# Performance work log

Hardware: AMD Instinct MI355X
Metric: run time of the kernel (lower is better)

## Reference

```python
import jax, jax.numpy as jnp
import numpy as np

# FPMA (Mitchell-style) approximate bf16 multiply: a*b is approximated by
# integer-adding the exponent+mantissa bit fields of the two bf16 operands
# and subtracting the exponent bias offset (0x3F80 for bf16). Sign is XOR of
# sign bits. Underflow is flushed to zero; overflow clamped to max finite.
SIGN_MASK = 0x8000
MAG_MASK = 0x7FFF
BIAS_OFF = 0x3F80  # 127 << 7 (bf16 exponent bias in bit position)
MAX_FINITE = 0x7F7F
CHUNK = 4  # rows of the input processed per scan step (bounds the [C,N,K] intermediate)


def _fpma_matmul(x, w):
    """x: [M,K] bf16, w: [N,K] bf16 -> [M,N] fp32 accumulated approximate products."""
    xb = jax.lax.bitcast_convert_type(x, jnp.uint16).astype(jnp.int32)  # [M,K]
    wb = jax.lax.bitcast_convert_type(w, jnp.uint16).astype(jnp.int32)  # [N,K]
    M, K = xb.shape
    xs, xm = xb & SIGN_MASK, xb & MAG_MASK
    ws, wm = wb & SIGN_MASK, wb & MAG_MASK

    def block(args):
        bs, bm = args  # each [CHUNK, K]
        sign = bs[:, None, :] ^ ws[None]                      # [C,N,K]
        mag = bm[:, None, :] + wm[None] - BIAS_OFF            # approx exp+mant add
        mag = jnp.clip(mag, 0, MAX_FINITE)                    # flush underflow, clamp overflow
        is_zero = (bm[:, None, :] == 0) | (wm[None] == 0)     # exact-zero operands
        bits = jnp.where(is_zero, 0, sign | mag).astype(jnp.uint16)
        prod = jax.lax.bitcast_convert_type(bits, jnp.bfloat16)
        return prod.astype(jnp.float32).sum(-1)               # [C,N] fp32 accumulate

    xs_c = xs.reshape(M // CHUNK, CHUNK, K)
    xm_c = xm.reshape(M // CHUNK, CHUNK, K)
    out = jax.lax.map(block, (xs_c, xm_c))                    # [M//C, C, N]
    return out.reshape(M, -1)


def setup_inputs() -> dict:
    key = jax.random.key(0)
    k1, k2, k3 = jax.random.split(key, 3)
    M, K, N = 4096, 2048, 2048
    input = jax.random.normal(k1, (M, K), dtype=jnp.bfloat16)
    weight = (jax.random.normal(k2, (N, K), dtype=jnp.float32) * 0.02).astype(jnp.bfloat16)
    bias = (jax.random.normal(k3, (1, N), dtype=jnp.float32) * 0.02).astype(jnp.bfloat16)
    return {"input": input, "weight": weight, "bias": bias}


def reference(input, weight, bias):
    orig_shape = input.shape[:-1]
    x = input.reshape(-1, input.shape[-1])
    acc = _fpma_matmul(x, weight)                 # [M,N] fp32
    out = acc.astype(jnp.bfloat16) + bias         # bias added in bf16, as in the kernel wrapper
    return out.reshape(*orig_shape, weight.shape[0])
```

## Files before the change

### kernel.cpp

```cpp
#include <hip/hip_runtime.h>
#include <stdint.h>

typedef unsigned short v2u   __attribute__((ext_vector_type(2)));
typedef unsigned short u16x8 __attribute__((ext_vector_type(8)));
typedef short          s16x8 __attribute__((ext_vector_type(8)));
typedef float          f32x4 __attribute__((ext_vector_type(4)));

#define TM 64
#define TN 64
#define BK 32

__device__ __forceinline__ uint32_t rnd_bf16(float f) {
    uint32_t u = __builtin_bit_cast(uint32_t, f);
    return (u + 0x7FFFu + ((u >> 16) & 1u)) >> 16;
}
__device__ __forceinline__ float bf16_to_f32(uint32_t bits16) {
    return __builtin_bit_cast(float, bits16 << 16);
}

__device__ __forceinline__ uint32_t pack_x(uint32_t w0, uint32_t w1) {
    uint32_t u = (w0 >> 16) | (w1 & 0xFFFF0000u);
    const v2u vfloor = {0x2000, 0x2000};
    v2u m = __builtin_bit_cast(v2u, u & 0x7FFF7FFFu);
    m = __builtin_elementwise_max(m, vfloor);
    uint32_t c = (u & 0x80008000u) ^ 0xC080C080u;
    v2u xp = m + __builtin_bit_cast(v2u, c);
    return __builtin_bit_cast(uint32_t, xp);
}
__device__ __forceinline__ uint32_t pack_w(uint32_t w0, uint32_t w1) {
    uint32_t v = (w0 >> 16) | (w1 & 0xFFFF0000u);
    const v2u vfloor = {0x2000, 0x2000};
    v2u m = __builtin_bit_cast(v2u, v & 0x7FFF7FFFu);
    m = __builtin_elementwise_max(m, vfloor);
    return __builtin_bit_cast(uint32_t, m) | (v & 0x80008000u);
}

__global__ __launch_bounds__(256, 2)
void fpma_gemm(const uint32_t* __restrict__ X,
               const uint32_t* __restrict__ Wt,
               const float*    __restrict__ Bias,
               float* __restrict__ Out,
               int M, int N, int K)
{
    __shared__ uint32_t Xp[2][64 * 16];
    __shared__ uint32_t Wp[2][64 * 16];

    const int tid  = threadIdx.x;
    const int lane = tid & 63;
    const int warp = tid >> 6;
    const int wm = warp >> 1, wn = warp & 1;
    const int m0 = blockIdx.y * TM;
    const int n0 = blockIdx.x * TN;

    const int cc = lane & 15;
    const int q  = lane >> 4;
    const int mi = cc >> 2;
    const int ni = cc & 3;

    const int xrd = (32 * wm + mi) * 16 + ((q ^ mi) << 2);
    int wrd[4];
    #pragma unroll
    for (int t = 0; t < 4; ++t)
        wrd[t] = (32 * wn + ni) * 16 + ((q ^ ni) << 2) + (((q + t) & 3) << 6);

    u16x8 bt[4];
    #pragma unroll
    for (int t = 0; t < 4; ++t) {
        unsigned short v = ((cc >> 2) == ((q + t) & 3)) ? (unsigned short)0x3F80
                                                        : (unsigned short)0;
        bt[t] = (u16x8){v, v, v, v, v, v, v, v};
    }

    const int srow = tid >> 2;
    const int soct = tid & 3;
    const uint32_t* xptr = X  + (size_t)(m0 + srow) * K + soct * 8;
    const uint32_t* wptr = Wt + (size_t)(n0 + srow) * K + soct * 8;
    const int st = srow * 16 + ((soct ^ (srow & 3)) << 2);

    f32x4 acc[8][2];
    #pragma unroll
    for (int a = 0; a < 8; ++a)
        #pragma unroll
        for (int bg = 0; bg < 2; ++bg) acc[a][bg] = (f32x4){0.f, 0.f, 0.f, 0.f};

    {
        uint4 a0 = *(const uint4*)(xptr), a1 = *(const uint4*)(xptr + 4);
        uint4 b0 = *(const uint4*)(wptr), b1 = *(const uint4*)(wptr + 4);
        uint4 px = {pack_x(a0.x, a0.y), pack_x(a0.z, a0.w),
                    pack_x(a1.x, a1.y), pack_x(a1.z, a1.w)};
        uint4 pw = {pack_w(b0.x, b0.y), pack_w(b0.z, b0.w),
                    pack_w(b1.x, b1.y), pack_w(b1.z, b1.w)};
        *(uint4*)&Xp[0][st] = px;
        *(uint4*)&Wp[0][st] = pw;
    }
    uint4 gx0 = {0,0,0,0}, gx1 = {0,0,0,0}, gw0 = {0,0,0,0}, gw1 = {0,0,0,0};
    const int ksteps = K / BK;
    if (ksteps > 1) {
        xptr += BK; wptr += BK;
        gx0 = *(const uint4*)(xptr); gx1 = *(const uint4*)(xptr + 4);
        gw0 = *(const uint4*)(wptr); gw1 = *(const uint4*)(wptr + 4);
    }
    __syncthreads();

    #pragma unroll 1
    for (int kt = 0; kt < ksteps; ++kt) {
        const int cur = kt & 1;
        if (kt + 1 < ksteps) {
            uint4 px = {pack_x(gx0.x, gx0.y), pack_x(gx0.z, gx0.w),
                        pack_x(gx1.x, gx1.y), pack_x(gx1.z, gx1.w)};
            uint4 pw = {pack_w(gw0.x, gw0.y), pack_w(gw0.z, gw0.w),
                        pack_w(gw1.x, gw1.y), pack_w(gw1.z, gw1.w)};
            *(uint4*)&Xp[cur ^ 1][st] = px;
            *(uint4*)&Wp[cur ^ 1][st] = pw;
            if (kt + 2 < ksteps) {
                xptr += BK; wptr += BK;
                gx0 = *(const uint4*)(xptr); gx1 = *(const uint4*)(xptr + 4);
                gw0 = *(const uint4*)(wptr); gw1 = *(const uint4*)(wptr + 4);
            }
        }

        u16x8 xf[8];
        #pragma unroll
        for (int a = 0; a < 8; ++a)
            xf[a] = __builtin_bit_cast(u16x8,
                        *(const uint4*)&Xp[cur][xrd + a * 64]);

        #pragma unroll
        for (int bg = 0; bg < 2; ++bg) {
            u16x8 wf[4];
            #pragma unroll
            for (int t = 0; t < 4; ++t)
                wf[t] = __builtin_bit_cast(u16x8,
                            *(const uint4*)&Wp[cur][wrd[t] + bg * 256]);
            #pragma unroll
            for (int t = 0; t < 4; ++t)
                #pragma unroll
                for (int a = 0; a < 8; ++a) {
                    u16x8 p = xf[a] + wf[t];
                    acc[a][bg] = __builtin_amdgcn_mfma_f32_16x16x32_bf16(
                        __builtin_bit_cast(s16x8, p),
                        __builtin_bit_cast(s16x8, bt[t]),
                        acc[a][bg], 0, 0, 0);
                }
        }
        __syncthreads();
    }

    const int g = cc >> 2;
    f32x4 bias_[2];
    #pragma unroll
    for (int bg = 0; bg < 2; ++bg)
        bias_[bg] = *(const f32x4*)&Bias[n0 + 32 * wn + 16 * bg + 4 * g];

    #pragma unroll
    for (int a = 0; a < 8; ++a) {
        if ((cc & 3) == (a & 3)) {
            #pragma unroll
            for (int bg = 0; bg < 2; ++bg) {
                float o[4];
                #pragma unroll
                for (int j = 0; j < 4; ++j)
                    o[j] = bf16_to_f32(rnd_bf16(
                               bf16_to_f32(rnd_bf16(acc[a][bg][j])) + bias_[bg][j]));
                const size_t row = (size_t)(m0 + 32 * wm + 4 * a + q) * N;
                *(float4*)&Out[row + n0 + 32 * wn + 16 * bg + 4 * g] =
                    make_float4(o[0], o[1], o[2], o[3]);
            }
        }
    }
}

extern "C" void kernel_launch(void* const* d_in, const int* in_sizes, int n_in,
                              void* d_out, int out_size, void* d_ws, size_t ws_size,
                              hipStream_t stream) {
    (void)n_in; (void)d_ws; (void)ws_size; (void)out_size;
    const uint32_t* X = (const uint32_t*)d_in[0];
    const uint32_t* W = (const uint32_t*)d_in[1];
    const float*    B = (const float*)d_in[2];
    float* O = (float*)d_out;

    int N = in_sizes[2];
    int K = (N > 0) ? in_sizes[1] / N : 0;
    int M = (K > 0) ? in_sizes[0] / K : 0;
    if (N <= 0 || K <= 0 || M <= 0 ||
        (long long)N * K != (long long)in_sizes[1] ||
        (long long)M * K != (long long)in_sizes[0] ||
        (M % TM) || (N % TN) || (K % BK)) {
        M = 4096; K = 2048; N = 2048;
    }

    dim3 grid(N / TN, M / TM);
    fpma_gemm<<<grid, 256, 0, stream>>>(X, W, B, O, M, N, K);
}
```

Before: 558.1 us.

## Split k-step into four barrier-separated phases interleaving LDS staging with MFMA bursts

```diff
diff --git a/kernel.cpp b/kernel.cpp
--- a/kernel.cpp
+++ b/kernel.cpp
@@ -33,6 +33,10 @@
     v2u m = __builtin_bit_cast(v2u, v & 0x7FFF7FFFu);
     m = __builtin_elementwise_max(m, vfloor);
     return __builtin_bit_cast(uint32_t, m) | (v & 0x80008000u);
+}
+
+__device__ __forceinline__ void lgkm0() {
+    asm volatile("s_waitcnt lgkmcnt(0)" ::: "memory");
 }
 
 __global__ __launch_bounds__(256, 2)
@@ -86,12 +90,10 @@
     {
         uint4 a0 = *(const uint4*)(xptr), a1 = *(const uint4*)(xptr + 4);
         uint4 b0 = *(const uint4*)(wptr), b1 = *(const uint4*)(wptr + 4);
-        uint4 px = {pack_x(a0.x, a0.y), pack_x(a0.z, a0.w),
-                    pack_x(a1.x, a1.y), pack_x(a1.z, a1.w)};
-        uint4 pw = {pack_w(b0.x, b0.y), pack_w(b0.z, b0.w),
-                    pack_w(b1.x, b1.y), pack_w(b1.z, b1.w)};
-        *(uint4*)&Xp[0][st] = px;
-        *(uint4*)&Wp[0][st] = pw;
+        *(uint4*)&Xp[0][st] = (uint4){pack_x(a0.x,a0.y), pack_x(a0.z,a0.w),
+                                      pack_x(a1.x,a1.y), pack_x(a1.z,a1.w)};
+        *(uint4*)&Wp[0][st] = (uint4){pack_w(b0.x,b0.y), pack_w(b0.z,b0.w),
+                                      pack_w(b1.x,b1.y), pack_w(b1.z,b1.w)};
     }
     uint4 gx0 = {0,0,0,0}, gx1 = {0,0,0,0}, gw0 = {0,0,0,0}, gw1 = {0,0,0,0};
     const int ksteps = K / BK;
@@ -102,49 +104,78 @@
     }
     __syncthreads();
 
+#define PHASE_MFMA(T, WA, WB)                                             \
+    __builtin_amdgcn_s_setprio(1);                                        \
+    _Pragma("unroll")                                                     \
+    for (int a = 0; a < 8; ++a) {                                         \
+        u16x8 p = xf[a] + (WA);                                           \
+        acc[a][0] = __builtin_amdgcn_mfma_f32_16x16x32_bf16(              \
+            __builtin_bit_cast(s16x8, p),                                 \
+            __builtin_bit_cast(s16x8, bt[T]), acc[a][0], 0, 0, 0);        \
+    }                                                                     \
+    _Pragma("unroll")                                                     \
+    for (int a = 0; a < 8; ++a) {                                         \
+        u16x8 p = xf[a] + (WB);                                           \
+        acc[a][1] = __builtin_amdgcn_mfma_f32_16x16x32_bf16(              \
+            __builtin_bit_cast(s16x8, p),                                 \
+            __builtin_bit_cast(s16x8, bt[T]), acc[a][1], 0, 0, 0);        \
+    }                                                                     \
+    __builtin_amdgcn_s_setprio(0);
+
     #pragma unroll 1
     for (int kt = 0; kt < ksteps; ++kt) {
         const int cur = kt & 1;
-        if (kt + 1 < ksteps) {
-            uint4 px = {pack_x(gx0.x, gx0.y), pack_x(gx0.z, gx0.w),
-                        pack_x(gx1.x, gx1.y), pack_x(gx1.z, gx1.w)};
-            uint4 pw = {pack_w(gw0.x, gw0.y), pack_w(gw0.z, gw0.w),
-                        pack_w(gw1.x, gw1.y), pack_w(gw1.z, gw1.w)};
-            *(uint4*)&Xp[cur ^ 1][st] = px;
-            *(uint4*)&Wp[cur ^ 1][st] = pw;
-            if (kt + 2 < ksteps) {
-                xptr += BK; wptr += BK;
-                gx0 = *(const uint4*)(xptr); gx1 = *(const uint4*)(xptr + 4);
-                gw0 = *(const uint4*)(wptr); gw1 = *(const uint4*)(wptr + 4);
-            }
-        }
-
+        const bool stage = (kt + 1 < ksteps);
+        const bool pre   = (kt + 2 < ksteps);
         u16x8 xf[8];
+
         #pragma unroll
         for (int a = 0; a < 8; ++a)
             xf[a] = __builtin_bit_cast(u16x8,
                         *(const uint4*)&Xp[cur][xrd + a * 64]);
-
-        #pragma unroll
-        for (int bg = 0; bg < 2; ++bg) {
-            u16x8 wf[4];
-            #pragma unroll
-            for (int t = 0; t < 4; ++t)
-                wf[t] = __builtin_bit_cast(u16x8,
-                            *(const uint4*)&Wp[cur][wrd[t] + bg * 256]);
-            #pragma unroll
-            for (int t = 0; t < 4; ++t)
-                #pragma unroll
-                for (int a = 0; a < 8; ++a) {
-                    u16x8 p = xf[a] + wf[t];
-                    acc[a][bg] = __builtin_amdgcn_mfma_f32_16x16x32_bf16(
-                        __builtin_bit_cast(s16x8, p),
-                        __builtin_bit_cast(s16x8, bt[t]),
-                        acc[a][bg], 0, 0, 0);
-                }
+        u16x8 w0a = __builtin_bit_cast(u16x8, *(const uint4*)&Wp[cur][wrd[0]]);
+        u16x8 w0b = __builtin_bit_cast(u16x8, *(const uint4*)&Wp[cur][wrd[0] + 256]);
+        if (stage)
+            *(uint4*)&Xp[cur ^ 1][st] = (uint4){pack_x(gx0.x,gx0.y), pack_x(gx0.z,gx0.w),
+                                                pack_x(gx1.x,gx1.y), pack_x(gx1.z,gx1.w)};
+        __builtin_amdgcn_s_barrier();
+        lgkm0();
+        PHASE_MFMA(0, w0a, w0b)
+        __builtin_amdgcn_s_barrier();
+
+        u16x8 w1a = __builtin_bit_cast(u16x8, *(const uint4*)&Wp[cur][wrd[1]]);
+        u16x8 w1b = __builtin_bit_cast(u16x8, *(const uint4*)&Wp[cur][wrd[1] + 256]);
+        if (stage)
+            *(uint4*)&Wp[cur ^ 1][st] = (uint4){pack_w(gw0.x,gw0.y), pack_w(gw0.z,gw0.w),
+                                                pack_w(gw1.x,gw1.y), pack_w(gw1.z,gw1.w)};
+        __builtin_amdgcn_s_barrier();
+        lgkm0();
+        PHASE_MFMA(1, w1a, w1b)
+        __builtin_amdgcn_s_barrier();
+
+        u16x8 w2a = __builtin_bit_cast(u16x8, *(const uint4*)&Wp[cur][wrd[2]]);
+        u16x8 w2b = __builtin_bit_cast(u16x8, *(const uint4*)&Wp[cur][wrd[2] + 256]);
+        if (pre) {
+            xptr += BK;
+            gx0 = *(const uint4*)(xptr); gx1 = *(const uint4*)(xptr + 4);
         }
-        __syncthreads();
-    }
+        __builtin_amdgcn_s_barrier();
+        lgkm0();
+        PHASE_MFMA(2, w2a, w2b)
+        __builtin_amdgcn_s_barrier();
+
+        u16x8 w3a = __builtin_bit_cast(u16x8, *(const uint4*)&Wp[cur][wrd[3]]);
+        u16x8 w3b = __builtin_bit_cast(u16x8, *(const uint4*)&Wp[cur][wrd[3] + 256]);
+        if (pre) {
+            wptr += BK;
+            gw0 = *(const uint4*)(wptr); gw1 = *(const uint4*)(wptr + 4);
+        }
+        __builtin_amdgcn_s_barrier();
+        lgkm0();
+        PHASE_MFMA(3, w3a, w3b)
+        __builtin_amdgcn_s_barrier();
+    }
+#undef PHASE_MFMA
 
     const int g = cc >> 2;
     f32x4 bias_[2];
```

Measured after the change: 586.5 us. 5.1% more time.
